# Kernel optimization log

Hardware: AMD Instinct MI355X
Metric: run time of the kernel (lower is better)

The kernel has to match this reference:

```python
import jax, jax.numpy as jnp
import numpy as np

L = 3          # num_legs
D = 32         # leg_dim == out_leg_dim (output_dim = input_dim = D**L)
NUM_NODES = 6  # num_levels * (num_legs - 1) = 3 * 2
B = 256        # batch


def setup_inputs() -> dict:
    key = jax.random.key(0)
    k1, k2 = jax.random.split(key, 2)
    inputs = jax.random.normal(k1, (B, D ** L), dtype=jnp.float32)
    # all 6 entangler nodes share shape (D,D,D,D) since leg_dim == out_leg_dim;
    # scale ~ 1/D to mimic glorot and keep the 6-contraction chain numerically sane
    nodes = jax.random.normal(k2, (NUM_NODES, D, D, D, D), dtype=jnp.float32) / D
    bias = jnp.zeros((D ** L,), dtype=jnp.float32)
    return {"inputs": inputs, "nodes": nodes, "bias": bias}


def reference(inputs, nodes, bias):
    # Faithful port of DenseEntangler.call: reshape the input vector to L legs,
    # then contract NUM_NODES 4-leg tensors; node i eats edge slots (i%L, (i+1)%L)
    # with its axes (0,1) and replaces them with its axes (2,3).
    # jnp.tensordot output axis order (free axes of x in order, then node axes 2,3)
    # matches tn.contract_between's default ordering, so the final flatten is identical.
    Bn = inputs.shape[0]
    x = inputs.reshape((Bn,) + (D,) * L)   # axis 0 = batch, axes 1..L = legs
    pos = list(range(1, L + 1))            # edge slot k -> current axis of x
    for i in range(NUM_NODES):
        s0, s1 = i % L, (i + 1) % L
        p, q = pos[s0], pos[s1]
        x = jnp.tensordot(x, nodes[i], axes=[[p, q], [0, 1]])
        # remaining axes of x keep order (batch stays axis 0); new node axes go last
        new_pos = [0] * L
        for k in range(L):
            if k == s0:
                new_pos[k] = L - 1
            elif k == s1:
                new_pos[k] = L
            else:
                a = pos[k]
                new_pos[k] = a - (p < a) - (q < a)
        pos = new_pos
    out = x.reshape(Bn, -1) + bias  # flatten in current axis order, as in the TF code
    return jax.nn.relu(out)
```

## Files before the change

### kernel.cpp

```cpp
#include <hip/hip_runtime.h>
#include <hip/hip_bf16.h>
#include <stdint.h>

using bf16 = __hip_bfloat16;
typedef __attribute__((ext_vector_type(8))) short short8;
typedef __attribute__((ext_vector_type(4))) float floatx4;

#define DD 32
#define DL3 32768
#define BATCH 256
#define NK 1024

__device__ __forceinline__ void load16(const void* g, void* l) {
  __builtin_amdgcn_global_load_lds((const __attribute__((address_space(1))) void*)g,
                                   (__attribute__((address_space(3))) void*)l,
                                   16, 0, 0);
}

__global__ __launch_bounds__(256) void prep_x(const float* __restrict__ x, bf16* __restrict__ dst) {
  int b = blockIdx.x >> 5, v = blockIdx.x & 31;
  __shared__ float tile[32][33];
  const float* xb = x + (size_t)b * DL3 + v * DD;
  int t = threadIdx.x;
#pragma unroll
  for (int it = 0; it < 4; ++it) {
    int u = (t >> 5) + it * 8, f = t & 31;
    tile[u][f] = xb[u * NK + f];
  }
  __syncthreads();
  bf16* db = dst + (size_t)b * DL3 + v * NK;
#pragma unroll
  for (int it = 0; it < 4; ++it) {
    int f = (t >> 5) + it * 8, u = t & 31;
    db[f * DD + u] = __float2bfloat16(tile[u][f]);
  }
}

__global__ __launch_bounds__(256) void prep_nodes(const float* __restrict__ nodes, bf16* __restrict__ dst) {
  int id = blockIdx.x;
  int nb = id & 31, kb = (id >> 5) & 31, i = id >> 10;
  const float* src = nodes + (size_t)i * 1048576;
  bf16* d = dst + (size_t)i * 1048576;
  __shared__ float tile[32][33];
  int t = threadIdx.x;
#pragma unroll
  for (int it = 0; it < 4; ++it) {
    int u = (t >> 5) + it * 8, j = t & 31;
    tile[u][j] = src[(size_t)(u * 32 + kb) * 1024 + nb * 32 + j];
  }
  __syncthreads();
#pragma unroll
  for (int it = 0; it < 4; ++it) {
    int j = (t >> 5) + it * 8, u = t & 31;
    d[(size_t)(nb * 32 + j) * 1024 + kb * 32 + u] = __float2bfloat16(tile[u][j]);
  }
}

template <bool FINAL>
__global__ __launch_bounds__(256, 4) void entangler_gemm(
    const bf16* __restrict__ A, const bf16* __restrict__ Bn,
    bf16* __restrict__ Cb, float* __restrict__ Cf, const float* __restrict__ bias) {
  __shared__ bf16 sA[2 * 64 * 32];
  __shared__ bf16 sB[2 * 128 * 32];
  const int t = threadIdx.x;
  const int lane = t & 63;
  const int lane16 = lane & 15, quad = lane >> 4;
  const int w = t >> 6;
  const int m0 = (w & 1) * 32, n0 = (w >> 1) * 64;
  const int b0 = blockIdx.x * 2;
  const int N0 = blockIdx.y * 128;

  floatx4 acc[2][4];
#pragma unroll
  for (int i = 0; i < 2; ++i)
#pragma unroll
    for (int j = 0; j < 4; ++j)
      acc[i][j] = (floatx4){0.f, 0.f, 0.f, 0.f};

  const bf16* Ab = A + (size_t)b0 * DL3;
  const bf16* Bb = Bn + (size_t)N0 * NK;

  for (int kv = 0; kv < 16; ++kv) {
    __syncthreads();
#pragma unroll
    for (int r = 0; r < 2; ++r) {
      int e = (r * 256 + t) * 8;
      int kk = e >> 11, bb = (e >> 10) & 1, remA = e & 1023;
      load16(Ab + (size_t)bb * DL3 + (size_t)(kv * 2 + kk) * NK + remA, sA + e);
    }
#pragma unroll
    for (int r = 0; r < 4; ++r) {
      int e = (r * 256 + t) * 8;
      int kk = e >> 12, n = (e >> 5) & 127, u8 = e & 31;
      load16(Bb + (size_t)n * NK + kv * 64 + kk * 32 + u8, sB + e);
    }
    __syncthreads();

#pragma unroll
    for (int kk = 0; kk < 2; ++kk) {
      const bf16* pA = sA + kk * 2048;
      const bf16* pB = sB + kk * 4096;
      short8 af[2], bfr[4];
#pragma unroll
      for (int i = 0; i < 2; ++i)
        af[i] = *(const short8*)(pA + (m0 + i * 16 + lane16) * 32 + quad * 8);
#pragma unroll
      for (int j = 0; j < 4; ++j)
        bfr[j] = *(const short8*)(pB + (n0 + j * 16 + lane16) * 32 + quad * 8);
#pragma unroll
      for (int i = 0; i < 2; ++i)
#pragma unroll
        for (int j = 0; j < 4; ++j)
          acc[i][j] = __builtin_amdgcn_mfma_f32_16x16x32_bf16(af[i], bfr[j], acc[i][j], 0, 0, 0);
    }
  }

  const int R0 = blockIdx.x * 64;
#pragma unroll
  for (int i = 0; i < 2; ++i) {
#pragma unroll
    for (int j = 0; j < 4; ++j) {
#pragma unroll
      for (int r = 0; r < 4; ++r) {
        int row = R0 + m0 + i * 16 + quad * 4 + r;
        int col = N0 + n0 + j * 16 + lane16;
        if (FINAL) {
          float v = acc[i][j][r] + bias[(row & 31) * 1024 + col];
          Cf[(size_t)row * 1024 + col] = fmaxf(v, 0.f);
        } else {
          Cb[(size_t)row * 1024 + col] = __float2bfloat16(acc[i][j][r]);
        }
      }
    }
  }
}

extern "C" void kernel_launch(void* const* d_in, const int* in_sizes, int n_in,
                              void* d_out, int out_size, void* d_ws, size_t ws_size,
                              hipStream_t stream) {
  const float* x     = (const float*)d_in[0];
  const float* nodes = (const float*)d_in[1];
  const float* bias  = (const float*)d_in[2];
  float* out = (float*)d_out;

  bf16* buf0  = (bf16*)d_ws;
  bf16* buf1  = buf0 + (size_t)BATCH * DL3;
  bf16* nodeT = buf1 + (size_t)BATCH * DL3;

  prep_x<<<dim3(BATCH * 32), dim3(256), 0, stream>>>(x, buf0);
  prep_nodes<<<dim3(6 * 1024), dim3(256), 0, stream>>>(nodes, nodeT);

  dim3 grid(128, 8), blk(256);
  entangler_gemm<false><<<grid, blk, 0, stream>>>(buf0, nodeT + (size_t)0 * 1048576, buf1, nullptr, nullptr);
  entangler_gemm<false><<<grid, blk, 0, stream>>>(buf1, nodeT + (size_t)1 * 1048576, buf0, nullptr, nullptr);
  entangler_gemm<false><<<grid, blk, 0, stream>>>(buf0, nodeT + (size_t)2 * 1048576, buf1, nullptr, nullptr);
  entangler_gemm<false><<<grid, blk, 0, stream>>>(buf1, nodeT + (size_t)3 * 1048576, buf0, nullptr, nullptr);
  entangler_gemm<false><<<grid, blk, 0, stream>>>(buf0, nodeT + (size_t)4 * 1048576, buf1, nullptr, nullptr);
  entangler_gemm<true ><<<grid, blk, 0, stream>>>(buf1, nodeT + (size_t)5 * 1048576, nullptr, out, bias);
}
```

Baseline: 253.6 us.

## Fuse all six entangler contractions into one persistent per-batch kernel

Measured after the change: 455.9 us. +79.8%, slower.

```diff
diff --git a/kernel.cpp b/kernel.cpp
--- a/kernel.cpp
+++ b/kernel.cpp
@@ -6,34 +6,12 @@
 typedef __attribute__((ext_vector_type(8))) short short8;
 typedef __attribute__((ext_vector_type(4))) float floatx4;
 
-#define DD 32
 #define DL3 32768
 #define BATCH 256
 #define NK 1024
 
-__device__ __forceinline__ void load16(const void* g, void* l) {
-  __builtin_amdgcn_global_load_lds((const __attribute__((address_space(1))) void*)g,
-                                   (__attribute__((address_space(3))) void*)l,
-                                   16, 0, 0);
-}
-
-__global__ __launch_bounds__(256) void prep_x(const float* __restrict__ x, bf16* __restrict__ dst) {
-  int b = blockIdx.x >> 5, v = blockIdx.x & 31;
-  __shared__ float tile[32][33];
-  const float* xb = x + (size_t)b * DL3 + v * DD;
-  int t = threadIdx.x;
-#pragma unroll
-  for (int it = 0; it < 4; ++it) {
-    int u = (t >> 5) + it * 8, f = t & 31;
-    tile[u][f] = xb[u * NK + f];
-  }
-  __syncthreads();
-  bf16* db = dst + (size_t)b * DL3 + v * NK;
-#pragma unroll
-  for (int it = 0; it < 4; ++it) {
-    int f = (t >> 5) + it * 8, u = t & 31;
-    db[f * DD + u] = __float2bfloat16(tile[u][f]);
-  }
+__device__ __forceinline__ int swz(int n) {
+  return (n & ~24) | ((((n >> 3) ^ (n >> 6)) & 3) << 3);
 }
 
 __global__ __launch_bounds__(256) void prep_nodes(const float* __restrict__ nodes, bf16* __restrict__ dst) {
@@ -56,81 +34,96 @@
   }
 }
 
-template <bool FINAL>
-__global__ __launch_bounds__(256, 4) void entangler_gemm(
-    const bf16* __restrict__ A, const bf16* __restrict__ Bn,
-    bf16* __restrict__ Cb, float* __restrict__ Cf, const float* __restrict__ bias) {
-  __shared__ bf16 sA[2 * 64 * 32];
-  __shared__ bf16 sB[2 * 128 * 32];
+__global__ __launch_bounds__(512, 2) void entangler_fused(
+    const float* __restrict__ x, const bf16* __restrict__ nodeT,
+    const float* __restrict__ bias, float* __restrict__ out) {
+  __shared__ bf16 S[32 * 1024];
+  const int b = blockIdx.x;
   const int t = threadIdx.x;
   const int lane = t & 63;
   const int lane16 = lane & 15, quad = lane >> 4;
   const int w = t >> 6;
-  const int m0 = (w & 1) * 32, n0 = (w >> 1) * 64;
-  const int b0 = blockIdx.x * 2;
-  const int N0 = blockIdx.y * 128;
 
-  floatx4 acc[2][4];
+  {
+    const float4* xb4 = (const float4*)(x + (size_t)b * DL3);
 #pragma unroll
-  for (int i = 0; i < 2; ++i)
+    for (int c = 0; c < 16; ++c) {
+      float4 vl = xb4[c * 512 + t];
+      int g0 = (c * 512 + t) * 4;
+      const float* pv = (const float*)&vl;
 #pragma unroll
-    for (int j = 0; j < 4; ++j)
-      acc[i][j] = (floatx4){0.f, 0.f, 0.f, 0.f};
+      for (int e = 0; e < 4; ++e) {
+        int g = g0 + e;
+        int u = g >> 10, v = (g >> 5) & 31, f = g & 31;
+        S[v * 1024 + swz(f * 32 + u)] = __float2bfloat16(pv[e]);
+      }
+    }
+  }
+  __syncthreads();
 
-  const bf16* Ab = A + (size_t)b0 * DL3;
-  const bf16* Bb = Bn + (size_t)N0 * NK;
+  const int sa = ((quad ^ ((lane16 >> 1) & 3)) << 3);
 
-  for (int kv = 0; kv < 16; ++kv) {
-    __syncthreads();
+  for (int step = 0; step < 6; ++step) {
+    const bf16* Bl = nodeT + (size_t)step * (NK * NK)
+                   + (size_t)(w * 128 + lane16) * NK + quad * 8;
+
+    floatx4 acc[2][8];
 #pragma unroll
-    for (int r = 0; r < 2; ++r) {
-      int e = (r * 256 + t) * 8;
-      int kk = e >> 11, bb = (e >> 10) & 1, remA = e & 1023;
-      load16(Ab + (size_t)bb * DL3 + (size_t)(kv * 2 + kk) * NK + remA, sA + e);
+    for (int i = 0; i < 2; ++i)
+#pragma unroll
+      for (int j = 0; j < 8; ++j)
+        acc[i][j] = (floatx4){0.f, 0.f, 0.f, 0.f};
+
+    short8 bcur[8], bnxt[8];
+#pragma unroll
+    for (int j = 0; j < 8; ++j)
+      bcur[j] = *(const short8*)(Bl + j * 16 * NK);
+
+#pragma unroll 2
+    for (int kv = 0; kv < 32; ++kv) {
+      const int kvn = (kv + 1) & 31;
+#pragma unroll
+      for (int j = 0; j < 8; ++j)
+        bnxt[j] = *(const short8*)(Bl + j * 16 * NK + kvn * 32);
+
+      short8 af0 = *(const short8*)(S + kv * 1024 + lane16 * 32 + sa);
+      short8 af1 = *(const short8*)(S + kv * 1024 + (16 + lane16) * 32 + sa);
+#pragma unroll
+      for (int j = 0; j < 8; ++j) {
+        acc[0][j] = __builtin_amdgcn_mfma_f32_16x16x32_bf16(af0, bcur[j], acc[0][j], 0, 0, 0);
+        acc[1][j] = __builtin_amdgcn_mfma_f32_16x16x32_bf16(af1, bcur[j], acc[1][j], 0, 0, 0);
+      }
+#pragma unroll
+      for (int j = 0; j < 8; ++j) bcur[j] = bnxt[j];
     }
-#pragma unroll
-    for (int r = 0; r < 4; ++r) {
-      int e = (r * 256 + t) * 8;
-      int kk = e >> 12, n = (e >> 5) & 127, u8 = e & 31;
-      load16(Bb + (size_t)n * NK + kv * 64 + kk * 32 + u8, sB + e);
-    }
+
     __syncthreads();
 
-#pragma unroll
-    for (int kk = 0; kk < 2; ++kk) {
-      const bf16* pA = sA + kk * 2048;
-      const bf16* pB = sB + kk * 4096;
-      short8 af[2], bfr[4];
-#pragma unroll
-      for (int i = 0; i < 2; ++i)
-        af[i] = *(const short8*)(pA + (m0 + i * 16 + lane16) * 32 + quad * 8);
-#pragma unroll
-      for (int j = 0; j < 4; ++j)
-        bfr[j] = *(const short8*)(pB + (n0 + j * 16 + lane16) * 32 + quad * 8);
+    if (step < 5) {
 #pragma unroll
       for (int i = 0; i < 2; ++i)
 #pragma unroll
-        for (int j = 0; j < 4; ++j)
-          acc[i][j] = __builtin_amdgcn_mfma_f32_16x16x32_bf16(af[i], bfr[j], acc[i][j], 0, 0, 0);
-    }
-  }
-
-  const int R0 = blockIdx.x * 64;
+        for (int j = 0; j < 8; ++j)
 #pragma unroll
-  for (int i = 0; i < 2; ++i) {
+          for (int r = 0; r < 4; ++r) {
+            int v = i * 16 + quad * 4 + r;
+            int n = w * 128 + j * 16 + lane16;
+            S[v * 1024 + swz(n)] = __float2bfloat16(acc[i][j][r]);
+          }
+      __syncthreads();
+    } else {
+      float* ob = out + (size_t)b * DL3;
 #pragma unroll
-    for (int j = 0; j < 4; ++j) {
+      for (int i = 0; i < 2; ++i)
 #pragma unroll
-      for (int r = 0; r < 4; ++r) {
-        int row = R0 + m0 + i * 16 + quad * 4 + r;
-        int col = N0 + n0 + j * 16 + lane16;
-        if (FINAL) {
-          float v = acc[i][j][r] + bias[(row & 31) * 1024 + col];
-          Cf[(size_t)row * 1024 + col] = fmaxf(v, 0.f);
-        } else {
-          Cb[(size_t)row * 1024 + col] = __float2bfloat16(acc[i][j][r]);
-        }
-      }
+        for (int j = 0; j < 8; ++j)
+#pragma unroll
+          for (int r = 0; r < 4; ++r) {
+            int row = i * 16 + quad * 4 + r;
+            int col = w * 128 + j * 16 + lane16;
+            float vv = acc[i][j][r] + bias[row * 1024 + col];
+            ob[(size_t)row * 1024 + col] = fmaxf(vv, 0.f);
+          }
     }
   }
 }
@@ -143,18 +136,8 @@
   const float* bias  = (const float*)d_in[2];
   float* out = (float*)d_out;
 
-  bf16* buf0  = (bf16*)d_ws;
-  bf16* buf1  = buf0 + (size_t)BATCH * DL3;
-  bf16* nodeT = buf1 + (size_t)BATCH * DL3;
+  bf16* nodeT = (bf16*)d_ws;
 
-  prep_x<<<dim3(BATCH * 32), dim3(256), 0, stream>>>(x, buf0);
   prep_nodes<<<dim3(6 * 1024), dim3(256), 0, stream>>>(nodes, nodeT);
-
-  dim3 grid(128, 8), blk(256);
-  entangler_gemm<false><<<grid, blk, 0, stream>>>(buf0, nodeT + (size_t)0 * 1048576, buf1, nullptr, nullptr);
-  entangler_gemm<false><<<grid, blk, 0, stream>>>(buf1, nodeT + (size_t)1 * 1048576, buf0, nullptr, nullptr);
-  entangler_gemm<false><<<grid, blk, 0, stream>>>(buf0, nodeT + (size_t)2 * 1048576, buf1, nullptr, nullptr);
-  entangler_gemm<false><<<grid, blk, 0, stream>>>(buf1, nodeT + (size_t)3 * 1048576, buf0, nullptr, nullptr);
-  entangler_gemm<false><<<grid, blk, 0, stream>>>(buf0, nodeT + (size_t)4 * 1048576, buf1, nullptr, nullptr);
-  entangler_gemm<true ><<<grid, blk, 0, stream>>>(buf1, nodeT + (size_t)5 * 1048576, nullptr, out, bias);
+  entangler_fused<<<dim3(BATCH), dim3(512), 0, stream>>>(x, nodeT, bias, out);
 }
```
